# Performance work log

Measured on AMD Instinct MI355X. Metric: run time of the kernel, lower is better.

## Reference

```python
import jax, jax.numpy as jnp
import numpy as np
from math import factorial, sqrt

MAX_RADIUS = 5.0
NUM_BASIS = 10
N_ATOMS = 200_000
N_EDGES = 3_200_000
N_GRAPHS = 2000

# ---- real-basis Clebsch-Gordan (l x l -> l) coefficients, computed once ----

def _cg(j1, m1, j2, m2, j3, m3):
    if m1 + m2 != m3:
        return 0.0
    f = factorial
    pre = sqrt((2*j3+1) * f(j3+j1-j2) * f(j3-j1+j2) * f(j1+j2-j3) / f(j1+j2+j3+1))
    pre *= sqrt(f(j3+m3)*f(j3-m3)*f(j1-m1)*f(j1+m1)*f(j2-m2)*f(j2+m2))
    s = 0.0
    kmin = max(0, j2-j3-m1, j1-j3+m2)
    kmax = min(j1+j2-j3, j1-m1, j2+m2)
    for k in range(kmin, kmax+1):
        s += (-1)**k / (f(k)*f(j1+j2-j3-k)*f(j1-m1-k)*f(j2+m2-k)*f(j3-j2+m1+k)*f(j3-j1-m2+k))
    return pre * s

def _U_real(l):
    U = np.zeros((2*l+1, 2*l+1), dtype=np.complex128)
    U[l, l] = 1.0
    for m in range(1, l+1):
        U[l+m, l+m] = (-1)**m / sqrt(2)
        U[l+m, l-m] = 1.0 / sqrt(2)
        U[l-m, l-m] = 1j / sqrt(2)
        U[l-m, l+m] = -1j * (-1)**m / sqrt(2)
    return U

def _real_cg(l):
    n = 2*l+1
    Cc = np.zeros((n, n, n), dtype=np.complex128)
    for m1 in range(-l, l+1):
        for m2 in range(-l, l+1):
            for m3 in range(-l, l+1):
                Cc[m1+l, m2+l, m3+l] = _cg(l, m1, l, m2, l, m3)
    U = _U_real(l)
    Cr = np.einsum('ai,bj,ck,ijk->abc', U, U, U.conj(), Cc)
    if np.abs(Cr.imag).max() > np.abs(Cr.real).max():
        Cr = Cr / 1j
    Cr = Cr.real
    return Cr / np.linalg.norm(Cr)

_C1 = jnp.asarray(_real_cg(1), dtype=jnp.float32)  # [3,3,3]
_C2 = jnp.asarray(_real_cg(2), dtype=jnp.float32)  # [5,5,5]


def _edge_embedding(r):
    # soft_one_hot_linspace, basis='smooth_finite', cutoff=True
    values = jnp.linspace(0.0, MAX_RADIUS, NUM_BASIS + 2)[1:-1]
    step = MAX_RADIUS / (NUM_BASIS + 1)
    d = (r[:, None] - values) / step          # [E, NUM_BASIS]
    inside = jnp.abs(d) < 1.0
    denom = jnp.where(inside, 1.0 - d * d, 1.0)
    bump = 1.14136 * jnp.exp(2.0 - 2.0 / denom)
    return jnp.where(inside, bump, 0.0) * jnp.sqrt(float(NUM_BASIS))


def setup_inputs() -> dict:
    key = jax.random.key(0)
    ks = jax.random.split(key, 10)
    inp = {
        'H_s': jax.random.normal(ks[0], (N_ATOMS, 4), jnp.float32),
        'H_p': jax.random.normal(ks[1], (N_ATOMS, 3, 3, 3), jnp.float32),
        'H_d': jax.random.normal(ks[2], (N_ATOMS, 2, 5, 5), jnp.float32),
        'pos': jax.random.normal(ks[3], (N_ATOMS, 3), jnp.float32) * 2.0,
        'w_s': jax.random.normal(ks[4], (1,), jnp.float32),
        'w_p': jax.random.normal(ks[5], (1,), jnp.float32),
        'w_d': jax.random.normal(ks[6], (1,), jnp.float32),
        'edge_src': jax.random.randint(ks[7], (N_EDGES,), 0, N_ATOMS, jnp.int32),
        'edge_dst': jax.random.randint(ks[8], (N_EDGES,), 0, N_ATOMS, jnp.int32),
        'graph_ids': jax.random.randint(ks[9], (N_ATOMS,), 0, N_GRAPHS, jnp.int32),
        'num_graphs': N_GRAPHS,
    }
    return inp


def reference(H_s, H_p, H_d, pos, w_s, w_p, w_d, edge_src, edge_dst, graph_ids, num_graphs):
    N = H_s.shape[0]
    n_s, n_p, n_d = H_s.shape[1], H_p.shape[1], H_d.shape[1]

    # s channel: sequential 0e x 0e -> 0e tensor products == scalar product chain
    ts = jnp.prod(w_s[0] * H_s, axis=1)               # [N]
    s_feat = (ts * ts / float(n_s * n_s))[:, None]    # [N,1] gram / n_s^2

    def channel(C, Hblk, w, dim, n):
        # tensor_X = eye(dim); for each shell block: TP_l(tensor_X, H_block)
        t0 = jnp.broadcast_to(jnp.eye(dim, dtype=Hblk.dtype), (N, dim, dim))
        scale = w[0] * jnp.sqrt(float(dim))           # sqrt(2l+1) path norm
        def step(t, Hb):                              # t,Hb: [N,dim,dim]
            return scale * jnp.einsum('ijk,nbi,nbj->nbk', C, t, Hb), None
        t, _ = jax.lax.scan(step, t0, jnp.moveaxis(Hblk, 1, 0))
        gram = jnp.einsum('nbk,nck->nbc', t, t) / float(n * n)
        return gram.reshape(N, dim * dim)

    p_feat = channel(_C1, H_p, w_p, 3, n_p)           # [N,9]
    d_feat = channel(_C2, H_d, w_d, 5, n_d)           # [N,25]

    minimal_basis = jnp.concatenate([s_feat, p_feat, d_feat], axis=1)  # [N,35]

    edge_vec = pos[edge_dst] - pos[edge_src]          # [E,3]
    r = jnp.sqrt(jnp.sum(edge_vec * edge_vec, axis=1) + 1e-12)
    emb = _edge_embedding(r)                          # [E,NUM_BASIS]

    out = jax.ops.segment_sum(minimal_basis.sum(axis=1), graph_ids, num_segments=num_graphs)
    return out, emb
```

## Files before the change

kernel.cpp:

```cpp
#include <hip/hip_runtime.h>
#include <cstddef>

#define K_A 0.2390457218668787f
#define K_B 0.11952286093343936f
#define K_G 0.20701966780270626f

struct C2T {
    float v[5][5][5];
    constexpr C2T() : v{} {
        v[2][2][2] = -K_A;
        v[2][1][1] = -K_B; v[2][3][3] = -K_B; v[1][2][1] = -K_B;
        v[3][2][3] = -K_B; v[1][1][2] = -K_B; v[3][3][2] = -K_B;
        v[2][0][0] =  K_A; v[2][4][4] =  K_A; v[0][2][0] =  K_A;
        v[4][2][4] =  K_A; v[0][0][2] =  K_A; v[4][4][2] =  K_A;
        v[1][1][4] =  K_G; v[4][1][1] =  K_G; v[1][4][1] =  K_G;
        v[3][3][4] = -K_G; v[4][3][3] = -K_G; v[3][4][3] = -K_G;
        v[1][3][0] = -K_G; v[3][1][0] = -K_G; v[0][1][3] = -K_G;
        v[0][3][1] = -K_G; v[1][0][3] = -K_G; v[3][0][1] = -K_G;
    }
};
constexpr C2T C2c{};

__global__ __launch_bounds__(256) void zero_kernel(float* __restrict__ out, int n) {
    int i = blockIdx.x * blockDim.x + threadIdx.x;
    if (i < n) out[i] = 0.0f;
}

__global__ __launch_bounds__(256) void atom_kernel(
    const float* __restrict__ Hs, const float* __restrict__ Hp,
    const float* __restrict__ Hd, const int* __restrict__ gid,
    const float* __restrict__ wsp, const float* __restrict__ wpp,
    const float* __restrict__ wdp, float* __restrict__ out, int N)
{
    int n = blockIdx.x * blockDim.x + threadIdx.x;
    if (n >= N) return;
    const float ws = wsp[0], wp = wpp[0], wd = wdp[0];

    const float4 hs = *(const float4*)(Hs + (size_t)n * 4);
    const float ws2 = ws * ws;
    const float ts = (ws2 * ws2) * hs.x * hs.y * hs.z * hs.w;
    float total = ts * ts * (1.0f / 16.0f);

    {
        const float* hp = Hp + (size_t)n * 27;
        const float cp = -wp * 0.70710678118654752f;
        float t[3][3] = {{1,0,0},{0,1,0},{0,0,1}};
        #pragma unroll
        for (int s = 0; s < 3; s++) {
            #pragma unroll
            for (int b = 0; b < 3; b++) {
                const float h0 = hp[s*9 + b*3 + 0];
                const float h1 = hp[s*9 + b*3 + 1];
                const float h2 = hp[s*9 + b*3 + 2];
                const float c0 = t[b][1]*h2 - t[b][2]*h1;
                const float c1 = t[b][2]*h0 - t[b][0]*h2;
                const float c2 = t[b][0]*h1 - t[b][1]*h0;
                t[b][0] = cp * c0; t[b][1] = cp * c1; t[b][2] = cp * c2;
            }
        }
        const float u0 = t[0][0] + t[1][0] + t[2][0];
        const float u1 = t[0][1] + t[1][1] + t[2][1];
        const float u2 = t[0][2] + t[1][2] + t[2][2];
        total += (u0*u0 + u1*u1 + u2*u2) * (1.0f / 9.0f);
    }

    {
        const float* hd = Hd + (size_t)n * 50;
        const float sd = wd * 2.23606797749978969f;
        float u[5] = {0, 0, 0, 0, 0};
        #pragma unroll
        for (int b = 0; b < 5; b++) {
            float h0r[5], h1r[5], t1r[5];
            #pragma unroll
            for (int j = 0; j < 5; j++) h0r[j] = hd[b*5 + j];
            #pragma unroll
            for (int k = 0; k < 5; k++) {
                float acc = 0.0f;
                #pragma unroll
                for (int j = 0; j < 5; j++) acc += C2c.v[b][j][k] * h0r[j];
                t1r[k] = sd * acc;
            }
            #pragma unroll
            for (int j = 0; j < 5; j++) h1r[j] = hd[25 + b*5 + j];
            #pragma unroll
            for (int k = 0; k < 5; k++) {
                float acc = 0.0f;
                #pragma unroll
                for (int i = 0; i < 5; i++)
                    #pragma unroll
                    for (int j = 0; j < 5; j++)
                        acc += C2c.v[i][j][k] * (t1r[i] * h1r[j]);
                u[k] += sd * acc;
            }
        }
        total += (u[0]*u[0] + u[1]*u[1] + u[2]*u[2] + u[3]*u[3] + u[4]*u[4]) * 0.25f;
    }

    unsafeAtomicAdd(out + gid[n], total);
}

__global__ __launch_bounds__(256) void edge_kernel(
    const float* __restrict__ pos, const int* __restrict__ src,
    const int* __restrict__ dst, float* __restrict__ emb, int E)
{
    int e = blockIdx.x * blockDim.x + threadIdx.x;
    if (e >= E) return;
    const int s = src[e], d = dst[e];
    const float dx = pos[d*3 + 0] - pos[s*3 + 0];
    const float dy = pos[d*3 + 1] - pos[s*3 + 1];
    const float dz = pos[d*3 + 2] - pos[s*3 + 2];
    const float r = sqrtf(dx*dx + dy*dy + dz*dz + 1e-12f);
    const float rs = r * 2.2f;

    float o[10];
    #pragma unroll
    for (int q = 0; q < 10; q++) {
        const float dd = rs - (float)(q + 1);
        const float d2 = dd * dd;
        const bool inside = d2 < 1.0f;
        const float denom = inside ? (1.0f - d2) : 1.0f;
        const float b = (1.14136f * expf(2.0f - 2.0f / denom)) * 3.16227766016838f;
        o[q] = inside ? b : 0.0f;
    }

    float2* p2 = (float2*)(emb + (size_t)e * 10);
    p2[0] = make_float2(o[0], o[1]);
    p2[1] = make_float2(o[2], o[3]);
    p2[2] = make_float2(o[4], o[5]);
    p2[3] = make_float2(o[6], o[7]);
    p2[4] = make_float2(o[8], o[9]);
}

extern "C" void kernel_launch(void* const* d_in, const int* in_sizes, int n_in,
                              void* d_out, int out_size, void* d_ws, size_t ws_size,
                              hipStream_t stream) {
    const float* Hs  = (const float*)d_in[0];
    const float* Hp  = (const float*)d_in[1];
    const float* Hd  = (const float*)d_in[2];
    const float* pos = (const float*)d_in[3];
    const float* wsp = (const float*)d_in[4];
    const float* wpp = (const float*)d_in[5];
    const float* wdp = (const float*)d_in[6];
    const int* esrc  = (const int*)d_in[7];
    const int* edst  = (const int*)d_in[8];
    const int* gid   = (const int*)d_in[9];

    const int N = in_sizes[0] / 4;
    const int E = in_sizes[7];
    const int G = out_size - 10 * E;

    float* out = (float*)d_out;
    float* emb = out + G;

    zero_kernel<<<(G + 255) / 256, 256, 0, stream>>>(out, G);
    atom_kernel<<<(N + 255) / 256, 256, 0, stream>>>(Hs, Hp, Hd, gid, wsp, wpp, wdp, out, N);
    edge_kernel<<<(E + 255) / 256, 256, 0, stream>>>(pos, esrc, edst, emb, E);
}
```

Baseline: 107.0 us.

## Stage atom Hp/Hd through LDS and vectorize edge kernel with analytic bump

New measurement: 121.8 us. 13.9% more time.

```diff
diff --git a/kernel.cpp b/kernel.cpp
--- a/kernel.cpp
+++ b/kernel.cpp
@@ -32,17 +32,40 @@
     const float* __restrict__ wsp, const float* __restrict__ wpp,
     const float* __restrict__ wdp, float* __restrict__ out, int N)
 {
-    int n = blockIdx.x * blockDim.x + threadIdx.x;
-    if (n >= N) return;
+    __shared__ float lds[12800];
+    const int tid  = threadIdx.x;
+    const int base = blockIdx.x * 256;
+    const int nb   = min(256, N - base);
+    const bool active = tid < nb;
+    const int n = base + tid;
     const float ws = wsp[0], wp = wpp[0], wd = wdp[0];
 
-    const float4 hs = *(const float4*)(Hs + (size_t)n * 4);
-    const float ws2 = ws * ws;
-    const float ts = (ws2 * ws2) * hs.x * hs.y * hs.z * hs.w;
-    float total = ts * ts * (1.0f / 16.0f);
-
-    {
-        const float* hp = Hp + (size_t)n * 27;
+    float total = 0.0f;
+
+    if (active) {
+        const float4 hs = *(const float4*)(Hs + (size_t)n * 4);
+        const float ws2 = ws * ws;
+        const float ts = (ws2 * ws2) * hs.x * hs.y * hs.z * hs.w;
+        total = ts * ts * (1.0f / 16.0f);
+    }
+
+    if (nb == 256) {
+        const float4* gp4 = (const float4*)(Hp + (size_t)base * 27);
+        float4* l4 = (float4*)lds;
+        #pragma unroll
+        for (int k = 0; k < 7; k++) {
+            const int idx = tid + k * 256;
+            if (idx < 1728) l4[idx] = gp4[idx];
+        }
+    } else {
+        const float* gp = Hp + (size_t)base * 27;
+        const int tot = nb * 27;
+        for (int k = tid; k < tot; k += 256) lds[k] = gp[k];
+    }
+    __syncthreads();
+
+    if (active) {
+        const float* hp = lds + tid * 27;
         const float cp = -wp * 0.70710678118654752f;
         float t[3][3] = {{1,0,0},{0,1,0},{0,0,1}};
         #pragma unroll
@@ -63,9 +86,25 @@
         const float u2 = t[0][2] + t[1][2] + t[2][2];
         total += (u0*u0 + u1*u1 + u2*u2) * (1.0f / 9.0f);
     }
-
-    {
-        const float* hd = Hd + (size_t)n * 50;
+    __syncthreads();
+
+    if (nb == 256) {
+        const float4* gd4 = (const float4*)(Hd + (size_t)base * 50);
+        float4* l4 = (float4*)lds;
+        #pragma unroll
+        for (int k = 0; k < 13; k++) {
+            const int idx = tid + k * 256;
+            if (idx < 3200) l4[idx] = gd4[idx];
+        }
+    } else {
+        const float* gd = Hd + (size_t)base * 50;
+        const int tot = nb * 50;
+        for (int k = tid; k < tot; k += 256) lds[k] = gd[k];
+    }
+    __syncthreads();
+
+    if (active) {
+        const float* hd = lds + tid * 50;
         const float sd = wd * 2.23606797749978969f;
         float u[5] = {0, 0, 0, 0, 0};
         #pragma unroll
@@ -94,41 +133,82 @@
             }
         }
         total += (u[0]*u[0] + u[1]*u[1] + u[2]*u[2] + u[3]*u[3] + u[4]*u[4]) * 0.25f;
-    }
-
-    unsafeAtomicAdd(out + gid[n], total);
+        unsafeAtomicAdd(out + gid[n], total);
+    }
+}
+
+__device__ __forceinline__ float bumpf(float d) {
+    const float SC = 1.14136f * 3.16227766016838f;
+    const float denom = 1.0f - d * d;
+    const float inv = __builtin_amdgcn_rcpf(denom);
+    return SC * __expf(2.0f - 2.0f * inv);
 }
 
 __global__ __launch_bounds__(256) void edge_kernel(
     const float* __restrict__ pos, const int* __restrict__ src,
     const int* __restrict__ dst, float* __restrict__ emb, int E)
 {
-    int e = blockIdx.x * blockDim.x + threadIdx.x;
-    if (e >= E) return;
-    const int s = src[e], d = dst[e];
-    const float dx = pos[d*3 + 0] - pos[s*3 + 0];
-    const float dy = pos[d*3 + 1] - pos[s*3 + 1];
-    const float dz = pos[d*3 + 2] - pos[s*3 + 2];
-    const float r = sqrtf(dx*dx + dy*dy + dz*dz + 1e-12f);
-    const float rs = r * 2.2f;
-
-    float o[10];
-    #pragma unroll
-    for (int q = 0; q < 10; q++) {
-        const float dd = rs - (float)(q + 1);
-        const float d2 = dd * dd;
-        const bool inside = d2 < 1.0f;
-        const float denom = inside ? (1.0f - d2) : 1.0f;
-        const float b = (1.14136f * expf(2.0f - 2.0f / denom)) * 3.16227766016838f;
-        o[q] = inside ? b : 0.0f;
-    }
-
-    float2* p2 = (float2*)(emb + (size_t)e * 10);
-    p2[0] = make_float2(o[0], o[1]);
-    p2[1] = make_float2(o[2], o[3]);
-    p2[2] = make_float2(o[4], o[5]);
-    p2[3] = make_float2(o[6], o[7]);
-    p2[4] = make_float2(o[8], o[9]);
+    const int t = blockIdx.x * blockDim.x + threadIdx.x;
+    const int e0 = t * 4;
+    if (e0 >= E) return;
+    const float3* __restrict__ p3 = (const float3*)pos;
+
+    if (e0 + 3 < E) {
+        const int4 s4 = *(const int4*)(src + e0);
+        const int4 d4 = *(const int4*)(dst + e0);
+        const int ss[4] = {s4.x, s4.y, s4.z, s4.w};
+        const int dd[4] = {d4.x, d4.y, d4.z, d4.w};
+
+        float dx[4], dy[4], dz[4];
+        #pragma unroll
+        for (int u = 0; u < 4; u++) {
+            const float3 a = p3[ss[u]];
+            const float3 b = p3[dd[u]];
+            dx[u] = b.x - a.x; dy[u] = b.y - a.y; dz[u] = b.z - a.z;
+        }
+
+        float o[40];
+        #pragma unroll
+        for (int u = 0; u < 4; u++) {
+            const float r  = sqrtf(dx[u]*dx[u] + dy[u]*dy[u] + dz[u]*dz[u] + 1e-12f);
+            const float rs = r * 2.2f;
+            const float fq = floorf(rs);
+            const int   qa = (int)fq;
+            const float va = bumpf(rs - fq);
+            const float vb = bumpf(rs - fq - 1.0f);
+            #pragma unroll
+            for (int q = 0; q < 10; q++) {
+                float v = 0.0f;
+                v = (qa == q + 1) ? va : v;
+                v = (qa == q)     ? vb : v;
+                o[u*10 + q] = v;
+            }
+        }
+        float4* po = (float4*)(emb + (size_t)e0 * 10);
+        #pragma unroll
+        for (int k = 0; k < 10; k++)
+            po[k] = make_float4(o[k*4+0], o[k*4+1], o[k*4+2], o[k*4+3]);
+    } else {
+        for (int e = e0; e < E; e++) {
+            const int si = src[e], di = dst[e];
+            const float3 a = p3[si], b = p3[di];
+            const float ddx = b.x-a.x, ddy = b.y-a.y, ddz = b.z-a.z;
+            const float r  = sqrtf(ddx*ddx + ddy*ddy + ddz*ddz + 1e-12f);
+            const float rs = r * 2.2f;
+            const float fq = floorf(rs);
+            const int   qa = (int)fq;
+            const float va = bumpf(rs - fq);
+            const float vb = bumpf(rs - fq - 1.0f);
+            float* oe = emb + (size_t)e * 10;
+            #pragma unroll
+            for (int q = 0; q < 10; q++) {
+                float v = 0.0f;
+                v = (qa == q + 1) ? va : v;
+                v = (qa == q)     ? vb : v;
+                oe[q] = v;
+            }
+        }
+    }
 }
 
 extern "C" void kernel_launch(void* const* d_in, const int* in_sizes, int n_in,
@@ -154,5 +234,6 @@
 
     zero_kernel<<<(G + 255) / 256, 256, 0, stream>>>(out, G);
     atom_kernel<<<(N + 255) / 256, 256, 0, stream>>>(Hs, Hp, Hd, gid, wsp, wpp, wdp, out, N);
-    edge_kernel<<<(E + 255) / 256, 256, 0, stream>>>(pos, esrc, edst, emb, E);
-}
+    const int T = (E + 3) / 4;
+    edge_kernel<<<(T + 255) / 256, 256, 0, stream>>>(pos, esrc, edst, emb, E);
+}
```

## Pad positions to float4, evaluate only two bumps, stage edge output via LDS

Applied to the files above, without the earlier changes.

New measurement: 113.6 us. 6.2% more time.

```diff
diff --git a/kernel.cpp b/kernel.cpp
--- a/kernel.cpp
+++ b/kernel.cpp
@@ -1,5 +1,7 @@
 #include <hip/hip_runtime.h>
 #include <cstddef>
+
+typedef float floatx4 __attribute__((ext_vector_type(4)));
 
 #define K_A 0.2390457218668787f
 #define K_B 0.11952286093343936f
@@ -26,6 +28,14 @@
     if (i < n) out[i] = 0.0f;
 }
 
+__global__ __launch_bounds__(256) void pos4_kernel(
+    const float* __restrict__ pos, float4* __restrict__ pos4, int N)
+{
+    int i = blockIdx.x * blockDim.x + threadIdx.x;
+    if (i < N)
+        pos4[i] = make_float4(pos[3*i], pos[3*i+1], pos[3*i+2], 0.0f);
+}
+
 __global__ __launch_bounds__(256) void atom_kernel(
     const float* __restrict__ Hs, const float* __restrict__ Hp,
     const float* __restrict__ Hd, const int* __restrict__ gid,
@@ -99,36 +109,75 @@
     unsafeAtomicAdd(out + gid[n], total);
 }
 
+__device__ __forceinline__ float bumpf(float d) {
+    const float SC = 1.14136f * 3.16227766016838f;
+    const float denom = 1.0f - d * d;
+    const float inv = __builtin_amdgcn_rcpf(denom);
+    return SC * __expf(2.0f - 2.0f * inv);
+}
+
+template <int USE4>
 __global__ __launch_bounds__(256) void edge_kernel(
-    const float* __restrict__ pos, const int* __restrict__ src,
+    const void* __restrict__ posv, const int* __restrict__ src,
     const int* __restrict__ dst, float* __restrict__ emb, int E)
 {
-    int e = blockIdx.x * blockDim.x + threadIdx.x;
-    if (e >= E) return;
-    const int s = src[e], d = dst[e];
-    const float dx = pos[d*3 + 0] - pos[s*3 + 0];
-    const float dy = pos[d*3 + 1] - pos[s*3 + 1];
-    const float dz = pos[d*3 + 2] - pos[s*3 + 2];
-    const float r = sqrtf(dx*dx + dy*dy + dz*dz + 1e-12f);
-    const float rs = r * 2.2f;
-
-    float o[10];
-    #pragma unroll
-    for (int q = 0; q < 10; q++) {
-        const float dd = rs - (float)(q + 1);
-        const float d2 = dd * dd;
-        const bool inside = d2 < 1.0f;
-        const float denom = inside ? (1.0f - d2) : 1.0f;
-        const float b = (1.14136f * expf(2.0f - 2.0f / denom)) * 3.16227766016838f;
-        o[q] = inside ? b : 0.0f;
-    }
-
-    float2* p2 = (float2*)(emb + (size_t)e * 10);
-    p2[0] = make_float2(o[0], o[1]);
-    p2[1] = make_float2(o[2], o[3]);
-    p2[2] = make_float2(o[4], o[5]);
-    p2[3] = make_float2(o[6], o[7]);
-    p2[4] = make_float2(o[8], o[9]);
+    __shared__ float lds[256 * 11];
+    const int tid  = threadIdx.x;
+    const int base = blockIdx.x * 256;
+    const int nb   = min(256, E - base);
+    const int e    = base + tid;
+
+    if (tid < nb) {
+        const int s = __builtin_nontemporal_load(src + e);
+        const int d = __builtin_nontemporal_load(dst + e);
+        float dx, dy, dz;
+        if (USE4) {
+            const floatx4* p4 = (const floatx4*)posv;
+            const floatx4 a = p4[s];
+            const floatx4 b = p4[d];
+            dx = b.x - a.x; dy = b.y - a.y; dz = b.z - a.z;
+        } else {
+            const float* p = (const float*)posv;
+            dx = p[d*3+0] - p[s*3+0];
+            dy = p[d*3+1] - p[s*3+1];
+            dz = p[d*3+2] - p[s*3+2];
+        }
+        const float r  = sqrtf(dx*dx + dy*dy + dz*dz + 1e-12f);
+        const float rs = r * 2.2f;
+        const float fq = floorf(rs);
+        const int   qa = (int)fq;
+        const float va = bumpf(rs - fq);
+        const float vb = bumpf(rs - fq - 1.0f);
+        #pragma unroll
+        for (int q = 0; q < 10; q++) {
+            float v = 0.0f;
+            v = (qa == q + 1) ? va : v;
+            v = (qa == q)     ? vb : v;
+            lds[tid * 11 + q] = v;
+        }
+    }
+    __syncthreads();
+
+    float* outp = emb + (size_t)base * 10;
+    if (nb == 256) {
+        #pragma unroll
+        for (int it = 0; it < 3; it++) {
+            const int t4 = tid + it * 256;
+            if (t4 < 640) {
+                const int j = t4 * 4;
+                floatx4 v;
+                v.x = lds[((j+0)/10)*11 + (j+0)%10];
+                v.y = lds[((j+1)/10)*11 + (j+1)%10];
+                v.z = lds[((j+2)/10)*11 + (j+2)%10];
+                v.w = lds[((j+3)/10)*11 + (j+3)%10];
+                __builtin_nontemporal_store(v, (floatx4*)outp + t4);
+            }
+        }
+    } else {
+        const int tot = nb * 10;
+        for (int k = tid; k < tot; k += 256)
+            outp[k] = lds[(k/10)*11 + k%10];
+    }
 }
 
 extern "C" void kernel_launch(void* const* d_in, const int* in_sizes, int n_in,
@@ -153,6 +202,15 @@
     float* emb = out + G;
 
     zero_kernel<<<(G + 255) / 256, 256, 0, stream>>>(out, G);
-    atom_kernel<<<(N + 255) / 256, 256, 0, stream>>>(Hs, Hp, Hd, gid, wsp, wpp, wdp, out, N);
-    edge_kernel<<<(E + 255) / 256, 256, 0, stream>>>(pos, esrc, edst, emb, E);
-}
+
+    const bool use4 = ws_size >= (size_t)N * sizeof(float4);
+    if (use4) {
+        float4* pos4 = (float4*)d_ws;
+        pos4_kernel<<<(N + 255) / 256, 256, 0, stream>>>(pos, pos4, N);
+        atom_kernel<<<(N + 255) / 256, 256, 0, stream>>>(Hs, Hp, Hd, gid, wsp, wpp, wdp, out, N);
+        edge_kernel<1><<<(E + 255) / 256, 256, 0, stream>>>(pos4, esrc, edst, emb, E);
+    } else {
+        atom_kernel<<<(N + 255) / 256, 256, 0, stream>>>(Hs, Hp, Hd, gid, wsp, wpp, wdp, out, N);
+        edge_kernel<0><<<(E + 255) / 256, 256, 0, stream>>>(pos, esrc, edst, emb, E);
+    }
+}
```
